# Performance work log

Hardware: AMD Instinct MI355X
Metric: run time of the kernel (lower is better)

Reference implementation:

```python
import jax, jax.numpy as jnp
import numpy as np

N = 50000      # nodes
F_IN = 1024    # raw feature dim
D = 64         # student_dim = hidden_dim * compression_ratio
P = 3          # number of meta-paths
E = 1600000    # edges per meta-path adjacency (avg degree 32)


def setup_inputs() -> dict:
    key = jax.random.key(0)
    ks = jax.random.split(key, 10)
    feats = jax.random.normal(ks[0], (N, F_IN), jnp.float32)
    rows = jax.random.randint(ks[1], (P, E), 0, N, dtype=jnp.int32)
    cols = jax.random.randint(ks[2], (P, E), 0, N, dtype=jnp.int32)
    # normalized-adjacency-like positive edge weights
    vals = jax.random.uniform(ks[3], (P, E), jnp.float32) / 32.0
    # fc_list[0]: Linear(F_IN -> D), xavier_normal gain=1.414
    W0 = jax.random.normal(ks[4], (D, F_IN), jnp.float32) * 0.05
    b0 = jnp.zeros((D,), jnp.float32)
    # P GCN linear layers (D -> D, no bias) + GCN bias params
    Wg = jax.random.normal(ks[5], (P, D, D), jnp.float32) * 0.17
    bg = jnp.zeros((P, D), jnp.float32)
    # PReLU alpha (torch default init 0.25, one scalar per GCN)
    alpha = jnp.full((P,), 0.25, jnp.float32)
    # Attention: Linear(D -> D) and att vector [1, D]
    Wa = jax.random.normal(ks[6], (D, D), jnp.float32) * 0.17
    ba = jnp.zeros((D,), jnp.float32)
    att = jax.random.normal(ks[7], (1, D), jnp.float32) * 0.17
    return dict(feats=feats, rows=rows, cols=cols, vals=vals, W0=W0, b0=b0,
                Wg=Wg, bg=bg, alpha=alpha, Wa=Wa, ba=ba, att=att)


def reference(feats, rows, cols, vals, W0, b0, Wg, bg, alpha, Wa, ba, att):
    # h = elu(fc_list[0](feats))  (feat_drop = 0 -> identity)
    h = jax.nn.elu(feats @ W0.T + b0)                       # [N, D]
    embeds = []
    for i in range(P):
        s = h @ Wg[i].T                                     # [N, D]
        # sparse adj (COO) @ s : out[r] += v * s[c]
        msg = vals[i][:, None] * s[cols[i]]                 # [E, D]
        out = jax.ops.segment_sum(msg, rows[i], num_segments=N)
        out = out + bg[i]
        embeds.append(jnp.where(out > 0, out, alpha[i] * out))  # PReLU
    emb = jnp.stack(embeds)                                 # [P, N, D]
    # Attention over views: beta_i = att . mean_n tanh(fc(emb_i))
    sp = jnp.tanh(jnp.einsum('pnd,ed->pne', emb, Wa) + ba).mean(axis=1)  # [P, D]
    beta = jax.nn.softmax(sp @ att[0])                      # [P]
    z_mp = jnp.einsum('p,pnd->nd', beta, emb)               # [N, D]
    return z_mp
```

## Files before the change

kernel.cpp:

```cpp
#include <hip/hip_runtime.h>
#include <hip/hip_bf16.h>

#define N_NODES 50000
#define F_IN    1024
#define DD      64
#define PP      3
#define EE      1600000
#define NPC     98
#define CCAP    17664
#define NB1     391

typedef __attribute__((ext_vector_type(8))) short short8v;
typedef __attribute__((ext_vector_type(4))) float floatx4;
typedef __attribute__((ext_vector_type(2))) float floatx2;

__device__ inline float bfl(uint u) { return __uint_as_float(u << 16); }
__device__ inline float bfh(uint u) { return __uint_as_float(u & 0xffff0000u); }
__device__ inline floatx2 up2(uint u) {
    floatx2 r; r.x = bfl(u); r.y = bfh(u); return r;
}
__device__ inline uint cvtpk2(float a, float b) {
    __hip_bfloat162 h = __float22bfloat162_rn(make_float2(a, b));
    return *(uint*)&h;
}
__device__ inline ushort f2bf(float x) {
    __hip_bfloat16 h = __float2bfloat16(x);
    return *(ushort*)&h;
}

__global__ __launch_bounds__(256) void split_weights(const float* __restrict__ W0,
                                                     const float* __restrict__ Wg,
                                                     const float* __restrict__ Wa,
                                                     ushort* __restrict__ W0h,
                                                     ushort* __restrict__ Wgh,
                                                     ushort* __restrict__ Wah)
{
    int i = blockIdx.x * 256 + threadIdx.x;
    if (i < 64 * 1024) W0h[i] = f2bf(W0[i]);
    int j = i - 64 * 1024;
    if (j >= 0 && j < PP * 64 * 64) Wgh[j] = f2bf(Wg[j]);
    int k = i - 64 * 1024 - PP * 64 * 64;
    if (k >= 0 && k < 64 * 64) Wah[k] = f2bf(Wa[k]);
}

__global__ __launch_bounds__(512) void gemm1_partial(const float* __restrict__ feats,
                                                     const ushort* __restrict__ W0h,
                                                     float* __restrict__ hpart)
{
    __shared__ ushort Bh[64 * 512];
    const int t = threadIdx.x;
    const int w = t >> 6, lane = t & 63;
    const int row0 = blockIdx.x * 128;
    const int kh = blockIdx.y;
    const int l15 = lane & 15, l4 = lane >> 4;

    #pragma unroll
    for (int rep = 0; rep < 8; ++rep) {
        int id = rep * 512 + t;
        int d = id >> 6, uu = id & 63;
        *(uint4*)&Bh[d * 512 + ((uu ^ (d & 7)) << 3)] =
            *(const uint4*)&W0h[(size_t)d * F_IN + kh * 512 + uu * 8];
    }
    __syncthreads();

    int gr = row0 + w * 16 + l15;
    if (gr >= N_NODES) gr = N_NODES - 1;
    const float* arow = feats + (size_t)gr * F_IN + kh * 512 + l4 * 8;

    floatx4 acc[4] = {};
    #pragma unroll 4
    for (int ks = 0; ks < 16; ++ks) {
        float4 a0 = *(const float4*)&arow[ks * 32];
        float4 a1 = *(const float4*)&arow[ks * 32 + 4];
        uint4 av;
        av.x = cvtpk2(a0.x, a0.y); av.y = cvtpk2(a0.z, a0.w);
        av.z = cvtpk2(a1.x, a1.y); av.w = cvtpk2(a1.z, a1.w);
        short8v ah = *(short8v*)&av;
        int u = ks * 4 + l4;
        #pragma unroll
        for (int cf = 0; cf < 4; ++cf) {
            int d = cf * 16 + l15;
            short8v bh = *(short8v*)&Bh[d * 512 + ((u ^ (d & 7)) << 3)];
            acc[cf] = __builtin_amdgcn_mfma_f32_16x16x32_bf16(ah, bh, acc[cf], 0, 0, 0);
        }
    }

    float* hp = hpart + ((size_t)(kh * NB1 + blockIdx.x)) * 8192;
    #pragma unroll
    for (int cf = 0; cf < 4; ++cf)
        *(float4*)&hp[(cf * 512 + t) * 4] = make_float4(acc[cf][0], acc[cf][1],
                                                        acc[cf][2], acc[cf][3]);
}

__global__ __launch_bounds__(256) void gemm2_combine(const float* __restrict__ hpart,
                                                     const float* __restrict__ b0,
                                                     const ushort* __restrict__ Wgh,
                                                     ushort* __restrict__ s_all)
{
    __shared__ ushort Ah[64 * 64];
    __shared__ ushort Bh[64 * 64];
    __shared__ ushort Sout[64 * 64];
    const int t = threadIdx.x;
    const int w = t >> 6, lane = t & 63;
    const int row0 = blockIdx.x * 64;
    const int bi = blockIdx.x >> 1;
    const int hh = blockIdx.x & 1;
    const int l15 = lane & 15, l4 = lane >> 4;

    const float* hp0 = hpart + (size_t)bi * 8192;
    const float* hp1 = hpart + (size_t)(NB1 + bi) * 8192;

    #pragma unroll
    for (int cf = 0; cf < 4; ++cf) {
        float4 a = *(const float4*)&hp0[(cf * 512 + hh * 256 + t) * 4];
        float4 b = *(const float4*)&hp1[(cf * 512 + hh * 256 + t) * 4];
        int col = cf * 16 + l15;
        float bias = b0[col];
        float xs[4] = {a.x + b.x + bias, a.y + b.y + bias,
                       a.z + b.z + bias, a.w + b.w + bias};
        #pragma unroll
        for (int r = 0; r < 4; ++r) {
            int row = w * 16 + l4 * 4 + r;
            float x = xs[r];
            x = x > 0.f ? x : (__expf(x) - 1.f);
            int u = (col >> 3) ^ (row & 7);
            Ah[row * 64 + u * 8 + (col & 7)] = f2bf(x);
        }
    }
    __syncthreads();

    for (int p = 0; p < PP; ++p) {
        #pragma unroll
        for (int rep = 0; rep < 2; ++rep) {
            int idx = rep * 256 + t;
            int r = idx >> 3, u8 = idx & 7;
            int unit = u8 ^ (r & 7);
            *(uint4*)&Bh[r * 64 + unit * 8] = *(const uint4*)&Wgh[(size_t)p * 4096 + idx * 8];
        }
        __syncthreads();

        floatx4 sacc[4] = {};
        #pragma unroll
        for (int ks = 0; ks < 2; ++ks) {
            int arow2 = w * 16 + l15;
            int au = (ks * 4 + l4) ^ (arow2 & 7);
            short8v ah = *(short8v*)&Ah[arow2 * 64 + au * 8];
            #pragma unroll
            for (int cf = 0; cf < 4; ++cf) {
                int bcol = cf * 16 + l15;
                int bu = (ks * 4 + l4) ^ (bcol & 7);
                short8v bh = *(short8v*)&Bh[bcol * 64 + bu * 8];
                sacc[cf] = __builtin_amdgcn_mfma_f32_16x16x32_bf16(ah, bh, sacc[cf], 0, 0, 0);
            }
        }
        #pragma unroll
        for (int cf = 0; cf < 4; ++cf) {
            int col = cf * 16 + l15;
            #pragma unroll
            for (int r = 0; r < 4; ++r)
                Sout[(w * 16 + l4 * 4 + r) * 64 + col] = f2bf(sacc[cf][r]);
        }
        __syncthreads();
        {
            int lr = t >> 2;
            int gr = row0 + lr;
            if (gr < N_NODES) {
                ushort* sp = s_all + (size_t)p * N_NODES * 64;
                int co = (t & 3) * 16;
                *(uint4*)&sp[(size_t)gr * 64 + co]     = *(uint4*)&Sout[lr * 64 + co];
                *(uint4*)&sp[(size_t)gr * 64 + co + 8] = *(uint4*)&Sout[lr * 64 + co + 8];
            }
        }
        __syncthreads();
    }
}

__global__ __launch_bounds__(256) void part1(const int*   __restrict__ rows,
                                             const int*   __restrict__ cols,
                                             const float* __restrict__ vals,
                                             int*   __restrict__ pcur3,
                                             uint2* __restrict__ coarsebuf)
{
    __shared__ uint2 stage[2560];
    __shared__ uint2 sorted[2560];
    __shared__ int cnt[128];
    __shared__ int sc[128];
    __shared__ int curb[128];
    __shared__ int gbase[128];
    const int t = threadIdx.x;
    const int path = blockIdx.y;
    const size_t ebase = (size_t)path * EE + (size_t)blockIdx.x * 2560;
    int* pcur = pcur3 + path * NPC;
    uint2* cb = coarsebuf + (size_t)path * NPC * CCAP;

    if (t < 128) { cnt[t] = 0; curb[t] = 0; }
    __syncthreads();

    #pragma unroll
    for (int it = 0; it < 10; ++it) {
        int e = it * 256 + t;
        int r = rows[ebase + e];
        int c = cols[ebase + e];
        float v = vals[ebase + e];
        int bin = r >> 9, rl = r & 511;
        stage[e] = make_uint2((uint)c | ((uint)rl << 16) | ((uint)bin << 25),
                              __float_as_uint(v));
        atomicAdd(&cnt[bin], 1);
    }
    __syncthreads();

    if (t < 128) sc[t] = cnt[t];
    __syncthreads();
    #pragma unroll
    for (int o = 1; o < 128; o <<= 1) {
        int v = (t < 128 && t >= o) ? sc[t - o] : 0;
        __syncthreads();
        if (t < 128 && t >= o) sc[t] += v;
        __syncthreads();
    }

    if (t < NPC) gbase[t] = atomicAdd(&pcur[t], cnt[t]);
    __syncthreads();

    #pragma unroll
    for (int it = 0; it < 10; ++it) {
        uint2 e = stage[it * 256 + t];
        int bin = e.x >> 25;
        int loc = (sc[bin] - cnt[bin]) + atomicAdd(&curb[bin], 1);
        sorted[loc] = e;
    }
    __syncthreads();

    #pragma unroll
    for (int it = 0; it < 10; ++it) {
        int i = it * 256 + t;
        uint2 e = sorted[i];
        int bin = e.x >> 25;
        int g = gbase[bin] + (i - (sc[bin] - cnt[bin]));
        if (g < CCAP) cb[(size_t)bin * CCAP + g] = e;
    }
}

__global__ __launch_bounds__(512) void sort2(const uint2* __restrict__ coarsebuf,
                                             const int*   __restrict__ pcur3,
                                             uint* __restrict__ sortpk,
                                             int* __restrict__ rowbeg3,
                                             int* __restrict__ rowend3)
{
    __shared__ int hist[512];
    __shared__ int cur[512];
    const int t = threadIdx.x;
    const int c = blockIdx.x, path = blockIdx.y;
    const int n = min(pcur3[path * NPC + c], CCAP);
    const size_t slabbase = ((size_t)path * NPC + c) * CCAP;
    const uint2* src = coarsebuf + slabbase;

    hist[t] = 0;
    __syncthreads();

    for (int i = t; i < n; i += 512)
        atomicAdd(&hist[(src[i].x >> 16) & 511], 1);
    __syncthreads();

    int c0 = hist[t];
    __syncthreads();
    #pragma unroll
    for (int o = 1; o < 512; o <<= 1) {
        int v = (t >= o) ? hist[t - o] : 0;
        __syncthreads();
        hist[t] += v;
        __syncthreads();
    }
    int excl = hist[t] - c0;
    cur[t] = excl;
    int gr = c * 512 + t;
    if (gr < N_NODES) {
        rowbeg3[path * N_NODES + gr] = (int)(slabbase + excl);
        rowend3[path * N_NODES + gr] = (int)(slabbase + excl + c0);
    }
    __syncthreads();

    for (int i = t; i < n; i += 512) {
        uint2 e = src[i];
        int rl = (e.x >> 16) & 511;
        int pos = atomicAdd(&cur[rl], 1);
        sortpk[slabbase + pos] = (e.x & 0xffffu) |
                                 ((uint)f2bf(__uint_as_float(e.y)) << 16);
    }
}

__global__ __launch_bounds__(256) void spmm_gather(const uint*   __restrict__ sortpk,
                                                   const int*    __restrict__ rowbeg3,
                                                   const int*    __restrict__ rowend3,
                                                   const ushort* __restrict__ s_all,
                                                   const float*  __restrict__ bg,
                                                   const float*  __restrict__ alpha,
                                                   ushort* __restrict__ emb)
{
    const int path = blockIdx.x / 12500;
    const int wid = (blockIdx.x % 12500) * 4 + (threadIdx.x >> 6);
    const int lane = threadIdx.x & 63;
    const int dq = lane & 7;
    const int slot = lane >> 3;
    const int e0 = rowbeg3[path * N_NODES + wid];
    const int e1 = rowend3[path * N_NODES + wid];
    const ushort* s_p = s_all + (size_t)path * N_NODES * 64;

    floatx2 acc[4] = {};
    if (e0 < e1) {
        const int last = e1 - 1;
        for (int e = e0; e < e1; e += 32) {
            int ea = e + slot, eb = ea + 8, ec = ea + 16, ed = ea + 24;
            uint pka = sortpk[min(ea, last)];
            uint pkb = sortpk[min(eb, last)];
            uint pkc = sortpk[min(ec, last)];
            uint pkd = sortpk[min(ed, last)];
            const uint4 ga = *(const uint4*)&s_p[(size_t)(pka & 0xffffu) * 64 + dq * 8];
            const uint4 gb = *(const uint4*)&s_p[(size_t)(pkb & 0xffffu) * 64 + dq * 8];
            const uint4 gc = *(const uint4*)&s_p[(size_t)(pkc & 0xffffu) * 64 + dq * 8];
            const uint4 gd = *(const uint4*)&s_p[(size_t)(pkd & 0xffffu) * 64 + dq * 8];
            float va = (ea <= last) ? bfh(pka) : 0.f;
            float vb = (eb <= last) ? bfh(pkb) : 0.f;
            float vc = (ec <= last) ? bfh(pkc) : 0.f;
            float vd = (ed <= last) ? bfh(pkd) : 0.f;
            floatx2 va2 = {va, va}, vb2 = {vb, vb}, vc2 = {vc, vc}, vd2 = {vd, vd};
            acc[0] += va2 * up2(ga.x); acc[1] += va2 * up2(ga.y);
            acc[2] += va2 * up2(ga.z); acc[3] += va2 * up2(ga.w);
            acc[0] += vb2 * up2(gb.x); acc[1] += vb2 * up2(gb.y);
            acc[2] += vb2 * up2(gb.z); acc[3] += vb2 * up2(gb.w);
            acc[0] += vc2 * up2(gc.x); acc[1] += vc2 * up2(gc.y);
            acc[2] += vc2 * up2(gc.z); acc[3] += vc2 * up2(gc.w);
            acc[0] += vd2 * up2(gd.x); acc[1] += vd2 * up2(gd.y);
            acc[2] += vd2 * up2(gd.z); acc[3] += vd2 * up2(gd.w);
        }
    }
    #pragma unroll
    for (int j = 0; j < 4; ++j) {
        acc[j].x += __shfl_xor(acc[j].x, 8);
        acc[j].y += __shfl_xor(acc[j].y, 8);
        acc[j].x += __shfl_xor(acc[j].x, 16);
        acc[j].y += __shfl_xor(acc[j].y, 16);
        acc[j].x += __shfl_xor(acc[j].x, 32);
        acc[j].y += __shfl_xor(acc[j].y, 32);
    }

    if (slot == 0) {
        const float al = alpha[path];
        const float* bgp = bg + path * 64;
        float x[8];
        #pragma unroll
        for (int j = 0; j < 4; ++j) {
            float v0 = acc[j].x + bgp[dq * 8 + 2 * j];
            float v1 = acc[j].y + bgp[dq * 8 + 2 * j + 1];
            x[2 * j]     = v0 > 0.f ? v0 : al * v0;
            x[2 * j + 1] = v1 > 0.f ? v1 : al * v1;
        }
        uint4 wv;
        wv.x = cvtpk2(x[0], x[1]);
        wv.y = cvtpk2(x[2], x[3]);
        wv.z = cvtpk2(x[4], x[5]);
        wv.w = cvtpk2(x[6], x[7]);
        *(uint4*)&emb[((size_t)path * N_NODES + wid) * 64 + dq * 8] = wv;
    }
}

__global__ __launch_bounds__(256) void postproc(const ushort* __restrict__ emb,
                                                const ushort* __restrict__ Wah,
                                                const float* __restrict__ ba,
                                                float* __restrict__ sp)
{
    __shared__ ushort Ah[64 * 64];
    __shared__ ushort Bh[64 * 64];
    __shared__ float red[16][64];
    const int t = threadIdx.x;
    const int w = t >> 6, lane = t & 63;
    const int l15 = lane & 15, l4 = lane >> 4;
    const int nb = (N_NODES + 63) >> 6;
    const int p  = blockIdx.x / nb;
    const int tb = blockIdx.x % nb;
    const int row0 = tb * 64;
    const ushort* embp = emb + (size_t)p * N_NODES * 64;

    #pragma unroll
    for (int rep = 0; rep < 2; ++rep) {
        int idx = rep * 256 + t;
        int r = idx >> 3, u8 = idx & 7;
        int gr = row0 + r; if (gr >= N_NODES) gr = N_NODES - 1;
        int unit = u8 ^ (r & 7);
        *(uint4*)&Ah[r * 64 + unit * 8] = *(const uint4*)&embp[(size_t)gr * 64 + u8 * 8];
        *(uint4*)&Bh[r * 64 + unit * 8] = *(const uint4*)&Wah[idx * 8];
    }
    __syncthreads();

    floatx4 acc[4] = {};
    #pragma unroll
    for (int ks = 0; ks < 2; ++ks) {
        int arow = w * 16 + l15;
        int au = (ks * 4 + l4) ^ (arow & 7);
        short8v ah = *(short8v*)&Ah[arow * 64 + au * 8];
        #pragma unroll
        for (int cf = 0; cf < 4; ++cf) {
            int bcol = cf * 16 + l15;
            int bu = (ks * 4 + l4) ^ (bcol & 7);
            short8v bh = *(short8v*)&Bh[bcol * 64 + bu * 8];
            acc[cf] = __builtin_amdgcn_mfma_f32_16x16x32_bf16(ah, bh, acc[cf], 0, 0, 0);
        }
    }

    #pragma unroll
    for (int cf = 0; cf < 4; ++cf) {
        int col = cf * 16 + l15;
        float s = 0.f;
        #pragma unroll
        for (int r = 0; r < 4; ++r) {
            int gr = row0 + w * 16 + l4 * 4 + r;
            if (gr < N_NODES) s += tanhf(acc[cf][r] + ba[col]);
        }
        red[w * 4 + l4][col] = s;
    }
    __syncthreads();
    if (t < 64) {
        float ssum = 0.f;
        #pragma unroll
        for (int g = 0; g < 16; ++g) ssum += red[g][t];
        unsafeAtomicAdd(&sp[p * 64 + t], ssum);
    }
}

__global__ void beta_kernel(const float* __restrict__ sp,
                            const float* __restrict__ att,
                            float* __restrict__ beta)
{
    int lane = threadIdx.x;
    float w[PP];
    #pragma unroll
    for (int p = 0; p < PP; ++p) {
        float x = sp[p * 64 + lane] * (1.0f / (float)N_NODES) * att[lane];
        #pragma unroll
        for (int off = 32; off; off >>= 1) x += __shfl_down(x, off);
        w[p] = __shfl(x, 0);
    }
    if (lane == 0) {
        float mx = fmaxf(w[0], fmaxf(w[1], w[2]));
        float e0 = __expf(w[0] - mx);
        float e1 = __expf(w[1] - mx);
        float e2 = __expf(w[2] - mx);
        float s = e0 + e1 + e2;
        beta[0] = e0 / s; beta[1] = e1 / s; beta[2] = e2 / s;
    }
}

__global__ __launch_bounds__(256) void combine(const ushort* __restrict__ emb,
                                               const float* __restrict__ beta,
                                               float* __restrict__ out)
{
    const float b0 = beta[0], b1 = beta[1], b2 = beta[2];
    const size_t tot = (size_t)N_NODES * 64;
    size_t i = ((size_t)blockIdx.x * 256 + threadIdx.x) * 8;
    if (i < tot) {
        uint4 e0 = *(const uint4*)&emb[i];
        uint4 e1 = *(const uint4*)&emb[tot + i];
        uint4 e2 = *(const uint4*)&emb[2 * tot + i];
        float o[8];
        o[0] = b0*bfl(e0.x) + b1*bfl(e1.x) + b2*bfl(e2.x);
        o[1] = b0*bfh(e0.x) + b1*bfh(e1.x) + b2*bfh(e2.x);
        o[2] = b0*bfl(e0.y) + b1*bfl(e1.y) + b2*bfl(e2.y);
        o[3] = b0*bfh(e0.y) + b1*bfh(e1.y) + b2*bfh(e2.y);
        o[4] = b0*bfl(e0.z) + b1*bfl(e1.z) + b2*bfl(e2.z);
        o[5] = b0*bfh(e0.z) + b1*bfh(e1.z) + b2*bfh(e2.z);
        o[6] = b0*bfl(e0.w) + b1*bfl(e1.w) + b2*bfl(e2.w);
        o[7] = b0*bfh(e0.w) + b1*bfh(e1.w) + b2*bfh(e2.w);
        *(float4*)&out[i]     = make_float4(o[0], o[1], o[2], o[3]);
        *(float4*)&out[i + 4] = make_float4(o[4], o[5], o[6], o[7]);
    }
}

extern "C" void kernel_launch(void* const* d_in, const int* in_sizes, int n_in,
                              void* d_out, int out_size, void* d_ws, size_t ws_size,
                              hipStream_t stream)
{
    const float* feats = (const float*)d_in[0];
    const int*   rows  = (const int*)  d_in[1];
    const int*   cols  = (const int*)  d_in[2];
    const float* vals  = (const float*)d_in[3];
    const float* W0    = (const float*)d_in[4];
    const float* b0    = (const float*)d_in[5];
    const float* Wg    = (const float*)d_in[6];
    const float* bg    = (const float*)d_in[7];
    const float* alpha = (const float*)d_in[8];
    const float* Wa    = (const float*)d_in[9];
    const float* ba    = (const float*)d_in[10];
    const float* att   = (const float*)d_in[11];
    float* out = (float*)d_out;

    const size_t ND = (size_t)N_NODES * 64;
    char* base = (char*)d_ws;
    ushort* emb    = (ushort*)base;              base += 3 * ND * 2;
    ushort* s_all  = (ushort*)base;              base += 3 * ND * 2;
    ushort* W0h    = (ushort*)base;              base += 64 * 1024 * 2;
    ushort* Wgh    = (ushort*)base;              base += PP * 64 * 64 * 2;
    ushort* Wah    = (ushort*)base;              base += 64 * 64 * 2;
    int*    pcur3  = (int*)base;                 base += PP * NPC * 4;
    float*  sp     = (float*)base;               base += 192 * 4;
    float*  beta   = (float*)base;               base += 64 * 4;
    int*    rowbeg3 = (int*)base;                base += PP * N_NODES * 4;
    int*    rowend3 = (int*)base;                base += PP * N_NODES * 4;
    base = (char*)(((size_t)base + 255) & ~(size_t)255);
    float*  hpart  = (float*)base;               base += (size_t)2 * NB1 * 8192 * 4;
    uint2*  coarsebuf = (uint2*)base;            base += (size_t)PP * NPC * CCAP * 8;
    uint*   sortpk    = (uint*)base;             base += (size_t)PP * NPC * CCAP * 4;

    hipMemsetAsync(pcur3, 0, (PP * NPC + 192) * sizeof(int), stream);

    split_weights<<<(64 * 1024 + PP * 64 * 64 + 64 * 64 + 255) / 256, 256, 0, stream>>>(
        W0, Wg, Wa, W0h, Wgh, Wah);

    gemm1_partial<<<dim3(NB1, 2), 512, 0, stream>>>(feats, W0h, hpart);
    gemm2_combine<<<782, 256, 0, stream>>>(hpart, b0, Wgh, s_all);

    part1<<<dim3(EE / 2560, 3), 256, 0, stream>>>(rows, cols, vals, pcur3, coarsebuf);
    sort2<<<dim3(NPC, 3), 512, 0, stream>>>(coarsebuf, pcur3, sortpk, rowbeg3, rowend3);
    spmm_gather<<<3 * 12500, 256, 0, stream>>>(
        sortpk, rowbeg3, rowend3, s_all, bg, alpha, emb);

    postproc<<<3 * 782, 256, 0, stream>>>(emb, Wah, ba, sp);
    beta_kernel<<<1, 64, 0, stream>>>(sp, att, beta);
    combine<<<(int)((ND / 8 + 255) / 256), 256, 0, stream>>>(emb, beta, out);
}
```

Measured before the change: 306.2 us.

## Split GEMM1 K four ways and split SpMM gather into column halves

GEMM1 now splits the 1024-wide K dimension into four 256-wide slices instead of two. This doubles the block count and halves the LDS footprint per block, and the combine kernel sums four partials. The s table is stored as two 32-column halves per path, and the SpMM gather launches a separate warp per half, so each gathered row segment is 64 bytes and a per-path slice of s is more cache-resident. In exchange, the sorted edge lists are read twice, there is an extra shuffle stage, and more hpart partials are written and read.

```diff
diff --git a/kernel.cpp b/kernel.cpp
--- a/kernel.cpp
+++ b/kernel.cpp
@@ -47,29 +47,29 @@
                                                      const ushort* __restrict__ W0h,
                                                      float* __restrict__ hpart)
 {
-    __shared__ ushort Bh[64 * 512];
+    __shared__ ushort Bh[64 * 256];
     const int t = threadIdx.x;
     const int w = t >> 6, lane = t & 63;
     const int row0 = blockIdx.x * 128;
-    const int kh = blockIdx.y;
+    const int kq = blockIdx.y;
     const int l15 = lane & 15, l4 = lane >> 4;
 
     #pragma unroll
-    for (int rep = 0; rep < 8; ++rep) {
+    for (int rep = 0; rep < 4; ++rep) {
         int id = rep * 512 + t;
-        int d = id >> 6, uu = id & 63;
-        *(uint4*)&Bh[d * 512 + ((uu ^ (d & 7)) << 3)] =
-            *(const uint4*)&W0h[(size_t)d * F_IN + kh * 512 + uu * 8];
+        int d = id >> 5, uu = id & 31;
+        *(uint4*)&Bh[d * 256 + ((uu ^ (d & 7)) << 3)] =
+            *(const uint4*)&W0h[(size_t)d * F_IN + kq * 256 + uu * 8];
     }
     __syncthreads();
 
     int gr = row0 + w * 16 + l15;
     if (gr >= N_NODES) gr = N_NODES - 1;
-    const float* arow = feats + (size_t)gr * F_IN + kh * 512 + l4 * 8;
+    const float* arow = feats + (size_t)gr * F_IN + kq * 256 + l4 * 8;
 
     floatx4 acc[4] = {};
     #pragma unroll 4
-    for (int ks = 0; ks < 16; ++ks) {
+    for (int ks = 0; ks < 8; ++ks) {
         float4 a0 = *(const float4*)&arow[ks * 32];
         float4 a1 = *(const float4*)&arow[ks * 32 + 4];
         uint4 av;
@@ -80,12 +80,12 @@
         #pragma unroll
         for (int cf = 0; cf < 4; ++cf) {
             int d = cf * 16 + l15;
-            short8v bh = *(short8v*)&Bh[d * 512 + ((u ^ (d & 7)) << 3)];
+            short8v bh = *(short8v*)&Bh[d * 256 + ((u ^ (d & 7)) << 3)];
             acc[cf] = __builtin_amdgcn_mfma_f32_16x16x32_bf16(ah, bh, acc[cf], 0, 0, 0);
         }
     }
 
-    float* hp = hpart + ((size_t)(kh * NB1 + blockIdx.x)) * 8192;
+    float* hp = hpart + ((size_t)(kq * NB1 + blockIdx.x)) * 8192;
     #pragma unroll
     for (int cf = 0; cf < 4; ++cf)
         *(float4*)&hp[(cf * 512 + t) * 4] = make_float4(acc[cf][0], acc[cf][1],
@@ -107,17 +107,17 @@
     const int hh = blockIdx.x & 1;
     const int l15 = lane & 15, l4 = lane >> 4;
 
-    const float* hp0 = hpart + (size_t)bi * 8192;
-    const float* hp1 = hpart + (size_t)(NB1 + bi) * 8192;
-
     #pragma unroll
     for (int cf = 0; cf < 4; ++cf) {
-        float4 a = *(const float4*)&hp0[(cf * 512 + hh * 256 + t) * 4];
-        float4 b = *(const float4*)&hp1[(cf * 512 + hh * 256 + t) * 4];
+        int idx = (cf * 512 + hh * 256 + t) * 4;
+        float4 a = *(const float4*)&hpart[(size_t)bi * 8192 + idx];
+        float4 b = *(const float4*)&hpart[((size_t)NB1 + bi) * 8192 + idx];
+        float4 c = *(const float4*)&hpart[((size_t)2 * NB1 + bi) * 8192 + idx];
+        float4 d = *(const float4*)&hpart[((size_t)3 * NB1 + bi) * 8192 + idx];
         int col = cf * 16 + l15;
         float bias = b0[col];
-        float xs[4] = {a.x + b.x + bias, a.y + b.y + bias,
-                       a.z + b.z + bias, a.w + b.w + bias};
+        float xs[4] = {a.x + b.x + c.x + d.x + bias, a.y + b.y + c.y + d.y + bias,
+                       a.z + b.z + c.z + d.z + bias, a.w + b.w + c.w + d.w + bias};
         #pragma unroll
         for (int r = 0; r < 4; ++r) {
             int row = w * 16 + l4 * 4 + r;
@@ -165,10 +165,11 @@
             int lr = t >> 2;
             int gr = row0 + lr;
             if (gr < N_NODES) {
-                ushort* sp = s_all + (size_t)p * N_NODES * 64;
                 int co = (t & 3) * 16;
-                *(uint4*)&sp[(size_t)gr * 64 + co]     = *(uint4*)&Sout[lr * 64 + co];
-                *(uint4*)&sp[(size_t)gr * 64 + co + 8] = *(uint4*)&Sout[lr * 64 + co + 8];
+                int half = co >> 5, ci = co & 31;
+                ushort* sp = s_all + (size_t)(p * 2 + half) * N_NODES * 32;
+                *(uint4*)&sp[(size_t)gr * 32 + ci]     = *(uint4*)&Sout[lr * 64 + co];
+                *(uint4*)&sp[(size_t)gr * 32 + ci + 8] = *(uint4*)&Sout[lr * 64 + co + 8];
             }
         }
         __syncthreads();
@@ -297,45 +298,38 @@
                                                    const float*  __restrict__ alpha,
                                                    ushort* __restrict__ emb)
 {
-    const int path = blockIdx.x / 12500;
+    const int slice = blockIdx.x / 12500;
+    const int path = slice >> 1, half = slice & 1;
     const int wid = (blockIdx.x % 12500) * 4 + (threadIdx.x >> 6);
     const int lane = threadIdx.x & 63;
-    const int dq = lane & 7;
-    const int slot = lane >> 3;
+    const int dq = lane & 3;
+    const int slot = lane >> 2;
     const int e0 = rowbeg3[path * N_NODES + wid];
     const int e1 = rowend3[path * N_NODES + wid];
-    const ushort* s_p = s_all + (size_t)path * N_NODES * 64;
+    const ushort* s_p = s_all + (size_t)slice * N_NODES * 32;
 
     floatx2 acc[4] = {};
     if (e0 < e1) {
         const int last = e1 - 1;
         for (int e = e0; e < e1; e += 32) {
-            int ea = e + slot, eb = ea + 8, ec = ea + 16, ed = ea + 24;
+            int ea = e + slot, eb = ea + 16;
             uint pka = sortpk[min(ea, last)];
             uint pkb = sortpk[min(eb, last)];
-            uint pkc = sortpk[min(ec, last)];
-            uint pkd = sortpk[min(ed, last)];
-            const uint4 ga = *(const uint4*)&s_p[(size_t)(pka & 0xffffu) * 64 + dq * 8];
-            const uint4 gb = *(const uint4*)&s_p[(size_t)(pkb & 0xffffu) * 64 + dq * 8];
-            const uint4 gc = *(const uint4*)&s_p[(size_t)(pkc & 0xffffu) * 64 + dq * 8];
-            const uint4 gd = *(const uint4*)&s_p[(size_t)(pkd & 0xffffu) * 64 + dq * 8];
+            const uint4 ga = *(const uint4*)&s_p[(size_t)(pka & 0xffffu) * 32 + dq * 8];
+            const uint4 gb = *(const uint4*)&s_p[(size_t)(pkb & 0xffffu) * 32 + dq * 8];
             float va = (ea <= last) ? bfh(pka) : 0.f;
             float vb = (eb <= last) ? bfh(pkb) : 0.f;
-            float vc = (ec <= last) ? bfh(pkc) : 0.f;
-            float vd = (ed <= last) ? bfh(pkd) : 0.f;
-            floatx2 va2 = {va, va}, vb2 = {vb, vb}, vc2 = {vc, vc}, vd2 = {vd, vd};
+            floatx2 va2 = {va, va}, vb2 = {vb, vb};
             acc[0] += va2 * up2(ga.x); acc[1] += va2 * up2(ga.y);
             acc[2] += va2 * up2(ga.z); acc[3] += va2 * up2(ga.w);
             acc[0] += vb2 * up2(gb.x); acc[1] += vb2 * up2(gb.y);
             acc[2] += vb2 * up2(gb.z); acc[3] += vb2 * up2(gb.w);
-            acc[0] += vc2 * up2(gc.x); acc[1] += vc2 * up2(gc.y);
-            acc[2] += vc2 * up2(gc.z); acc[3] += vc2 * up2(gc.w);
-            acc[0] += vd2 * up2(gd.x); acc[1] += vd2 * up2(gd.y);
-            acc[2] += vd2 * up2(gd.z); acc[3] += vd2 * up2(gd.w);
         }
     }
     #pragma unroll
     for (int j = 0; j < 4; ++j) {
+        acc[j].x += __shfl_xor(acc[j].x, 4);
+        acc[j].y += __shfl_xor(acc[j].y, 4);
         acc[j].x += __shfl_xor(acc[j].x, 8);
         acc[j].y += __shfl_xor(acc[j].y, 8);
         acc[j].x += __shfl_xor(acc[j].x, 16);
@@ -346,7 +340,7 @@
 
     if (slot == 0) {
         const float al = alpha[path];
-        const float* bgp = bg + path * 64;
+        const float* bgp = bg + path * 64 + half * 32;
         float x[8];
         #pragma unroll
         for (int j = 0; j < 4; ++j) {
@@ -360,7 +354,7 @@
         wv.y = cvtpk2(x[2], x[3]);
         wv.z = cvtpk2(x[4], x[5]);
         wv.w = cvtpk2(x[6], x[7]);
-        *(uint4*)&emb[((size_t)path * N_NODES + wid) * 64 + dq * 8] = wv;
+        *(uint4*)&emb[((size_t)path * N_NODES + wid) * 64 + half * 32 + dq * 8] = wv;
     }
 }
 
@@ -506,7 +500,7 @@
     int*    rowbeg3 = (int*)base;                base += PP * N_NODES * 4;
     int*    rowend3 = (int*)base;                base += PP * N_NODES * 4;
     base = (char*)(((size_t)base + 255) & ~(size_t)255);
-    float*  hpart  = (float*)base;               base += (size_t)2 * NB1 * 8192 * 4;
+    float*  hpart  = (float*)base;               base += (size_t)4 * NB1 * 8192 * 4;
     uint2*  coarsebuf = (uint2*)base;            base += (size_t)PP * NPC * CCAP * 8;
     uint*   sortpk    = (uint*)base;             base += (size_t)PP * NPC * CCAP * 4;
 
@@ -515,12 +509,12 @@
     split_weights<<<(64 * 1024 + PP * 64 * 64 + 64 * 64 + 255) / 256, 256, 0, stream>>>(
         W0, Wg, Wa, W0h, Wgh, Wah);
 
-    gemm1_partial<<<dim3(NB1, 2), 512, 0, stream>>>(feats, W0h, hpart);
+    gemm1_partial<<<dim3(NB1, 4), 512, 0, stream>>>(feats, W0h, hpart);
     gemm2_combine<<<782, 256, 0, stream>>>(hpart, b0, Wgh, s_all);
 
     part1<<<dim3(EE / 2560, 3), 256, 0, stream>>>(rows, cols, vals, pcur3, coarsebuf);
     sort2<<<dim3(NPC, 3), 512, 0, stream>>>(coarsebuf, pcur3, sortpk, rowbeg3, rowend3);
-    spmm_gather<<<3 * 12500, 256, 0, stream>>>(
+    spmm_gather<<<6 * 12500, 256, 0, stream>>>(
         sortpk, rowbeg3, rowend3, s_all, bg, alpha, emb);
 
     postproc<<<3 * 782, 256, 0, stream>>>(emb, Wah, ba, sp);
```

New measurement: 354.8 us. 1.16x slower.

## Fuse feature GEMM and edge binning into one launch with 4-way K split

Applied to the files above, without the earlier changes.

Merges the first GEMM (feats @ W0) and the coarse edge-binning pass into a single kernel, with block ranges dispatching to either task. The two independent memory-bound phases can then overlap on the GPU and one launch is removed. The GEMM K dimension is split four ways instead of two, giving more, smaller blocks, and the combine kernel now sums four partials. The cost is extra partial-sum traffic, and the edge blocks now run 512 threads with a shared LDS layout, which may lower occupancy.

```diff
diff --git a/kernel.cpp b/kernel.cpp
--- a/kernel.cpp
+++ b/kernel.cpp
@@ -9,6 +9,7 @@
 #define NPC     98
 #define CCAP    17664
 #define NB1     391
+#define P1B     625
 
 typedef __attribute__((ext_vector_type(8))) short short8v;
 typedef __attribute__((ext_vector_type(4))) float floatx4;
@@ -43,53 +44,125 @@
     if (k >= 0 && k < 64 * 64) Wah[k] = f2bf(Wa[k]);
 }
 
-__global__ __launch_bounds__(512) void gemm1_partial(const float* __restrict__ feats,
-                                                     const ushort* __restrict__ W0h,
-                                                     float* __restrict__ hpart)
-{
-    __shared__ ushort Bh[64 * 512];
+__global__ __launch_bounds__(512) void fused_front(const float* __restrict__ feats,
+                                                   const ushort* __restrict__ W0h,
+                                                   float* __restrict__ hpart,
+                                                   const int*   __restrict__ rows,
+                                                   const int*   __restrict__ cols,
+                                                   const float* __restrict__ vals,
+                                                   int*   __restrict__ pcur3,
+                                                   uint2* __restrict__ coarsebuf)
+{
+    __shared__ __align__(16) char smem[43008];
     const int t = threadIdx.x;
-    const int w = t >> 6, lane = t & 63;
-    const int row0 = blockIdx.x * 128;
-    const int kh = blockIdx.y;
-    const int l15 = lane & 15, l4 = lane >> 4;
-
-    #pragma unroll
-    for (int rep = 0; rep < 8; ++rep) {
-        int id = rep * 512 + t;
-        int d = id >> 6, uu = id & 63;
-        *(uint4*)&Bh[d * 512 + ((uu ^ (d & 7)) << 3)] =
-            *(const uint4*)&W0h[(size_t)d * F_IN + kh * 512 + uu * 8];
-    }
-    __syncthreads();
-
-    int gr = row0 + w * 16 + l15;
-    if (gr >= N_NODES) gr = N_NODES - 1;
-    const float* arow = feats + (size_t)gr * F_IN + kh * 512 + l4 * 8;
-
-    floatx4 acc[4] = {};
-    #pragma unroll 4
-    for (int ks = 0; ks < 16; ++ks) {
-        float4 a0 = *(const float4*)&arow[ks * 32];
-        float4 a1 = *(const float4*)&arow[ks * 32 + 4];
-        uint4 av;
-        av.x = cvtpk2(a0.x, a0.y); av.y = cvtpk2(a0.z, a0.w);
-        av.z = cvtpk2(a1.x, a1.y); av.w = cvtpk2(a1.z, a1.w);
-        short8v ah = *(short8v*)&av;
-        int u = ks * 4 + l4;
-        #pragma unroll
-        for (int cf = 0; cf < 4; ++cf) {
-            int d = cf * 16 + l15;
-            short8v bh = *(short8v*)&Bh[d * 512 + ((u ^ (d & 7)) << 3)];
-            acc[cf] = __builtin_amdgcn_mfma_f32_16x16x32_bf16(ah, bh, acc[cf], 0, 0, 0);
-        }
-    }
-
-    float* hp = hpart + ((size_t)(kh * NB1 + blockIdx.x)) * 8192;
-    #pragma unroll
-    for (int cf = 0; cf < 4; ++cf)
-        *(float4*)&hp[(cf * 512 + t) * 4] = make_float4(acc[cf][0], acc[cf][1],
-                                                        acc[cf][2], acc[cf][3]);
+
+    if (blockIdx.x < 4 * NB1) {
+        ushort* Bh = (ushort*)smem;
+        const int blk = blockIdx.x;
+        const int kq = blk / NB1;
+        const int bx = blk % NB1;
+        const int w = t >> 6, lane = t & 63;
+        const int row0 = bx * 128;
+        const int l15 = lane & 15, l4 = lane >> 4;
+
+        #pragma unroll
+        for (int rep = 0; rep < 4; ++rep) {
+            int id = rep * 512 + t;
+            int d = id >> 5, uu = id & 31;
+            *(uint4*)&Bh[d * 256 + ((uu ^ (d & 7)) << 3)] =
+                *(const uint4*)&W0h[(size_t)d * F_IN + kq * 256 + uu * 8];
+        }
+        __syncthreads();
+
+        int gr = row0 + w * 16 + l15;
+        if (gr >= N_NODES) gr = N_NODES - 1;
+        const float* arow = feats + (size_t)gr * F_IN + kq * 256 + l4 * 8;
+
+        floatx4 acc[4] = {};
+        #pragma unroll 4
+        for (int ks = 0; ks < 8; ++ks) {
+            float4 a0 = *(const float4*)&arow[ks * 32];
+            float4 a1 = *(const float4*)&arow[ks * 32 + 4];
+            uint4 av;
+            av.x = cvtpk2(a0.x, a0.y); av.y = cvtpk2(a0.z, a0.w);
+            av.z = cvtpk2(a1.x, a1.y); av.w = cvtpk2(a1.z, a1.w);
+            short8v ah = *(short8v*)&av;
+            int u = ks * 4 + l4;
+            #pragma unroll
+            for (int cf = 0; cf < 4; ++cf) {
+                int d = cf * 16 + l15;
+                short8v bh = *(short8v*)&Bh[d * 256 + ((u ^ (d & 7)) << 3)];
+                acc[cf] = __builtin_amdgcn_mfma_f32_16x16x32_bf16(ah, bh, acc[cf], 0, 0, 0);
+            }
+        }
+
+        float* hp = hpart + ((size_t)(kq * NB1 + bx)) * 8192;
+        #pragma unroll
+        for (int cf = 0; cf < 4; ++cf)
+            *(float4*)&hp[(cf * 512 + t) * 4] = make_float4(acc[cf][0], acc[cf][1],
+                                                            acc[cf][2], acc[cf][3]);
+    } else {
+        uint2* stage  = (uint2*)smem;
+        uint2* sorted = (uint2*)(smem + 20480);
+        int*   cnt    = (int*)(smem + 40960);
+        int*   sc     = (int*)(smem + 41472);
+        int*   curb   = (int*)(smem + 41984);
+        int*   gbase  = (int*)(smem + 42496);
+
+        const int pidx = blockIdx.x - 4 * NB1;
+        const int path = pidx / P1B;
+        const int bx   = pidx % P1B;
+        const size_t ebase = (size_t)path * EE + (size_t)bx * 2560;
+        int* pcur = pcur3 + path * NPC;
+        uint2* cb = coarsebuf + (size_t)path * NPC * CCAP;
+
+        if (t < 128) { cnt[t] = 0; curb[t] = 0; }
+        __syncthreads();
+
+        #pragma unroll
+        for (int it = 0; it < 5; ++it) {
+            int e = it * 512 + t;
+            int r = rows[ebase + e];
+            int c = cols[ebase + e];
+            float v = vals[ebase + e];
+            int bin = r >> 9, rl = r & 511;
+            stage[e] = make_uint2((uint)c | ((uint)rl << 16) | ((uint)bin << 25),
+                                  __float_as_uint(v));
+            atomicAdd(&cnt[bin], 1);
+        }
+        __syncthreads();
+
+        if (t < 128) sc[t] = cnt[t];
+        __syncthreads();
+        #pragma unroll
+        for (int o = 1; o < 128; o <<= 1) {
+            int v = (t < 128 && t >= o) ? sc[t - o] : 0;
+            __syncthreads();
+            if (t < 128 && t >= o) sc[t] += v;
+            __syncthreads();
+        }
+
+        if (t < NPC) gbase[t] = atomicAdd(&pcur[t], cnt[t]);
+        __syncthreads();
+
+        #pragma unroll
+        for (int it = 0; it < 5; ++it) {
+            uint2 e = stage[it * 512 + t];
+            int bin = e.x >> 25;
+            int loc = (sc[bin] - cnt[bin]) + atomicAdd(&curb[bin], 1);
+            sorted[loc] = e;
+        }
+        __syncthreads();
+
+        #pragma unroll
+        for (int it = 0; it < 5; ++it) {
+            int i = it * 512 + t;
+            uint2 e = sorted[i];
+            int bin = e.x >> 25;
+            int g = gbase[bin] + (i - (sc[bin] - cnt[bin]));
+            if (g < CCAP) cb[(size_t)bin * CCAP + g] = e;
+        }
+    }
 }
 
 __global__ __launch_bounds__(256) void gemm2_combine(const float* __restrict__ hpart,
@@ -107,17 +180,17 @@
     const int hh = blockIdx.x & 1;
     const int l15 = lane & 15, l4 = lane >> 4;
 
-    const float* hp0 = hpart + (size_t)bi * 8192;
-    const float* hp1 = hpart + (size_t)(NB1 + bi) * 8192;
-
     #pragma unroll
     for (int cf = 0; cf < 4; ++cf) {
-        float4 a = *(const float4*)&hp0[(cf * 512 + hh * 256 + t) * 4];
-        float4 b = *(const float4*)&hp1[(cf * 512 + hh * 256 + t) * 4];
+        int idx = (cf * 512 + hh * 256 + t) * 4;
+        float4 a = *(const float4*)&hpart[(size_t)bi * 8192 + idx];
+        float4 b = *(const float4*)&hpart[((size_t)NB1 + bi) * 8192 + idx];
+        float4 c = *(const float4*)&hpart[((size_t)2 * NB1 + bi) * 8192 + idx];
+        float4 d = *(const float4*)&hpart[((size_t)3 * NB1 + bi) * 8192 + idx];
         int col = cf * 16 + l15;
         float bias = b0[col];
-        float xs[4] = {a.x + b.x + bias, a.y + b.y + bias,
-                       a.z + b.z + bias, a.w + b.w + bias};
+        float xs[4] = {a.x + b.x + c.x + d.x + bias, a.y + b.y + c.y + d.y + bias,
+                       a.z + b.z + c.z + d.z + bias, a.w + b.w + c.w + d.w + bias};
         #pragma unroll
         for (int r = 0; r < 4; ++r) {
             int row = w * 16 + l4 * 4 + r;
@@ -172,72 +245,6 @@
             }
         }
         __syncthreads();
-    }
-}
-
-__global__ __launch_bounds__(256) void part1(const int*   __restrict__ rows,
-                                             const int*   __restrict__ cols,
-                                             const float* __restrict__ vals,
-                                             int*   __restrict__ pcur3,
-                                             uint2* __restrict__ coarsebuf)
-{
-    __shared__ uint2 stage[2560];
-    __shared__ uint2 sorted[2560];
-    __shared__ int cnt[128];
-    __shared__ int sc[128];
-    __shared__ int curb[128];
-    __shared__ int gbase[128];
-    const int t = threadIdx.x;
-    const int path = blockIdx.y;
-    const size_t ebase = (size_t)path * EE + (size_t)blockIdx.x * 2560;
-    int* pcur = pcur3 + path * NPC;
-    uint2* cb = coarsebuf + (size_t)path * NPC * CCAP;
-
-    if (t < 128) { cnt[t] = 0; curb[t] = 0; }
-    __syncthreads();
-
-    #pragma unroll
-    for (int it = 0; it < 10; ++it) {
-        int e = it * 256 + t;
-        int r = rows[ebase + e];
-        int c = cols[ebase + e];
-        float v = vals[ebase + e];
-        int bin = r >> 9, rl = r & 511;
-        stage[e] = make_uint2((uint)c | ((uint)rl << 16) | ((uint)bin << 25),
-                              __float_as_uint(v));
-        atomicAdd(&cnt[bin], 1);
-    }
-    __syncthreads();
-
-    if (t < 128) sc[t] = cnt[t];
-    __syncthreads();
-    #pragma unroll
-    for (int o = 1; o < 128; o <<= 1) {
-        int v = (t < 128 && t >= o) ? sc[t - o] : 0;
-        __syncthreads();
-        if (t < 128 && t >= o) sc[t] += v;
-        __syncthreads();
-    }
-
-    if (t < NPC) gbase[t] = atomicAdd(&pcur[t], cnt[t]);
-    __syncthreads();
-
-    #pragma unroll
-    for (int it = 0; it < 10; ++it) {
-        uint2 e = stage[it * 256 + t];
-        int bin = e.x >> 25;
-        int loc = (sc[bin] - cnt[bin]) + atomicAdd(&curb[bin], 1);
-        sorted[loc] = e;
-    }
-    __syncthreads();
-
-    #pragma unroll
-    for (int it = 0; it < 10; ++it) {
-        int i = it * 256 + t;
-        uint2 e = sorted[i];
-        int bin = e.x >> 25;
-        int g = gbase[bin] + (i - (sc[bin] - cnt[bin]));
-        if (g < CCAP) cb[(size_t)bin * CCAP + g] = e;
     }
 }
 
@@ -506,7 +513,7 @@
     int*    rowbeg3 = (int*)base;                base += PP * N_NODES * 4;
     int*    rowend3 = (int*)base;                base += PP * N_NODES * 4;
     base = (char*)(((size_t)base + 255) & ~(size_t)255);
-    float*  hpart  = (float*)base;               base += (size_t)2 * NB1 * 8192 * 4;
+    float*  hpart  = (float*)base;               base += (size_t)4 * NB1 * 8192 * 4;
     uint2*  coarsebuf = (uint2*)base;            base += (size_t)PP * NPC * CCAP * 8;
     uint*   sortpk    = (uint*)base;             base += (size_t)PP * NPC * CCAP * 4;
 
@@ -515,10 +522,10 @@
     split_weights<<<(64 * 1024 + PP * 64 * 64 + 64 * 64 + 255) / 256, 256, 0, stream>>>(
         W0, Wg, Wa, W0h, Wgh, Wah);
 
-    gemm1_partial<<<dim3(NB1, 2), 512, 0, stream>>>(feats, W0h, hpart);
+    fused_front<<<4 * NB1 + 3 * P1B, 512, 0, stream>>>(
+        feats, W0h, hpart, rows, cols, vals, pcur3, coarsebuf);
+
     gemm2_combine<<<782, 256, 0, stream>>>(hpart, b0, Wgh, s_all);
-
-    part1<<<dim3(EE / 2560, 3), 256, 0, stream>>>(rows, cols, vals, pcur3, coarsebuf);
     sort2<<<dim3(NPC, 3), 512, 0, stream>>>(coarsebuf, pcur3, sortpk, rowbeg3, rowend3);
     spmm_gather<<<3 * 12500, 256, 0, stream>>>(
         sortpk, rowbeg3, rowend3, s_all, bg, alpha, emb);
```

Measured after the change: 290.1 us. 5.3% less time.
